# Performance work log

Hardware: AMD Instinct MI355X
Metric: run time of the kernel (lower is better)

Reference implementation:

```python
import jax, jax.numpy as jnp
import numpy as np

LN_EPS = 1e-5

def _layernorm(x, w, b):
    mu = jnp.mean(x, axis=-1, keepdims=True)
    var = jnp.mean(jnp.square(x - mu), axis=-1, keepdims=True)
    return (x - mu) * jax.lax.rsqrt(var + LN_EPS) * w + b

def setup_inputs() -> dict:
    key = jax.random.key(0)
    ks = jax.random.split(key, 6)
    B, NQ, QD = 8, 576, 4096
    NKV, KVD = 2304, 1024
    s = 0.02
    return {
        "x_q": jax.random.normal(ks[0], (B, NQ, QD), jnp.float32),
        "x_kv": jax.random.normal(ks[1], (B, NKV, KVD), jnp.float32),
        "q_ln_w": jnp.ones((QD,), jnp.float32),
        "q_ln_b": jnp.zeros((QD,), jnp.float32),
        "q_w": jax.random.normal(ks[2], (QD, QD), jnp.float32) * s,
        "q_b": jnp.zeros((QD,), jnp.float32),
        "k_ln_w": jnp.ones((KVD,), jnp.float32),
        "k_ln_b": jnp.zeros((KVD,), jnp.float32),
        "k_w": jax.random.normal(ks[3], (KVD, QD), jnp.float32) * s,
        "k_b": jnp.zeros((QD,), jnp.float32),
        "v_ln_w": jnp.ones((KVD,), jnp.float32),
        "v_ln_b": jnp.zeros((KVD,), jnp.float32),
        "v_w": jax.random.normal(ks[4], (KVD, QD), jnp.float32) * s,
        "v_b": jnp.zeros((QD,), jnp.float32),
    }

def reference(x_q, x_kv, q_ln_w, q_ln_b, q_w, q_b,
              k_ln_w, k_ln_b, k_w, k_b, v_ln_w, v_ln_b, v_w, v_b):
    B, NQ, QD = x_q.shape
    hw = int(round(x_kv.shape[1] ** 0.5))          # 48
    KVD = x_kv.shape[-1]
    patch_num = int(round(NQ ** 0.5))              # 24
    patch_size = hw // patch_num                   # 2
    # 'b (h w) d -> b h w d' then group into patch_num x patch_num windows
    kv = x_kv.reshape(B, hw, hw, KVD)
    kv = kv.reshape(B, patch_num, patch_size, patch_num, patch_size, KVD)
    kv = kv.transpose(0, 1, 3, 2, 4, 5).reshape(B, patch_num * patch_num, patch_size * patch_size, KVD)
    # projections (LayerNorm + Linear)
    q = _layernorm(x_q, q_ln_w, q_ln_b) @ q_w + q_b            # [B, P2, QD]
    k = _layernorm(kv, k_ln_w, k_ln_b) @ k_w + k_b             # [B, P2, S2, QD]
    v = _layernorm(kv, v_ln_w, v_ln_b) @ v_w + v_b             # [B, P2, S2, QD]
    scale = 1.0 / (QD ** 0.5)
    att = jnp.einsum('bpd,bpsd->bps', q, k) * scale            # [B, P2, S2]
    att = jnp.nan_to_num(att)
    att = jax.nn.softmax(att, axis=-1)
    feat = jnp.einsum('bps,bpsd->bpd', att, v)                 # [B, P2, QD]
    return (x_q, feat)
```

## Files before the change

kernel.cpp:

```cpp
#include <hip/hip_runtime.h>
#include <cstdint>
#include <cstddef>


typedef __attribute__((ext_vector_type(8))) short short8;
typedef __attribute__((ext_vector_type(4))) float f32x4;

#define DEV __device__ __forceinline__

DEV unsigned short f2bf(float f) {
  union { float f; unsigned u; } x; x.f = f;
  unsigned r = x.u + 0x7fffu + ((x.u >> 16) & 1u);
  return (unsigned short)(r >> 16);
}
DEV float bf2f(unsigned short u) {
  union { unsigned u; float f; } x; x.u = ((unsigned)u) << 16;
  return x.f;
}

DEV void gload16(const void* g, void* l) {
  __builtin_amdgcn_global_load_lds(
      (const __attribute__((address_space(1))) unsigned int*)g,
      (__attribute__((address_space(3))) unsigned int*)l, 16, 0, 0);
}

template <bool PARTIAL, bool OUT_BF16, bool HAS_BIAS>
__global__ __launch_bounds__(256, 2) void gemm_nt(
    const unsigned short* __restrict__ A, const unsigned short* __restrict__ Bm,
    void* __restrict__ Cv, const float* __restrict__ bias, int M, int N,
    int Kfull, int Kchunk) {
  __shared__ __align__(16) unsigned short lds_a[128 * 64];
  __shared__ __align__(16) unsigned short lds_b[128 * 64];
  const int t = threadIdx.x;
  const int l = t & 63;
  const int w = t >> 6;

  int bx = blockIdx.x, by = blockIdx.y;
  {
    const int nbx = gridDim.x, nby = gridDim.y;
    const int nwg = nbx * nby;
    int flat = by * nbx + bx;
    flat = (flat & 7) * (nwg >> 3) + (flat >> 3);
    bx = flat % nbx;
    by = flat / nbx;
  }
  const long brow = (long)bx * 128;
  const long bcol = (long)by * 128;
  const int z = blockIdx.z;
  const int k0 = z * Kchunk;

  const int srow0 = t >> 3;
  const int gsrc = (t & 7) ^ ((t >> 3) & 7);
  const unsigned short* aS[4];
  const unsigned short* bS[4];
  unsigned short* aD[4];
  unsigned short* bD[4];
#pragma unroll
  for (int j = 0; j < 4; ++j) {
    const long row = srow0 + 32 * j;
    aS[j] = A + (brow + row) * (long)Kfull + k0 + gsrc * 8;
    bS[j] = Bm + (bcol + row) * (long)Kfull + k0 + gsrc * 8;
    aD[j] = lds_a + (t + 256 * j) * 8;
    bD[j] = lds_b + (t + 256 * j) * 8;
  }

  const int wr = w >> 1, wc = w & 1;
  const int fr = l & 15;
  const int xr = fr & 7;
  const int gq0 = l >> 4;

  f32x4 acc[4][4] = {};

  for (int kt = 0; kt < Kchunk; kt += 64) {
    __syncthreads();
#pragma unroll
    for (int j = 0; j < 4; ++j) {
      gload16(aS[j] + kt, aD[j]);
      gload16(bS[j] + kt, bD[j]);
    }
    asm volatile("s_waitcnt vmcnt(0)" ::: "memory");
    __syncthreads();
#pragma unroll
    for (int ks = 0; ks < 2; ++ks) {
      const int gx = ((ks * 4 + gq0) ^ xr) * 8;
      short8 af[4], bfr[4];
#pragma unroll
      for (int mi = 0; mi < 4; ++mi)
        af[mi] = *(const short8*)&lds_a[(wr * 64 + mi * 16 + fr) * 64 + gx];
#pragma unroll
      for (int ni = 0; ni < 4; ++ni)
        bfr[ni] = *(const short8*)&lds_b[(wc * 64 + ni * 16 + fr) * 64 + gx];
#pragma unroll
      for (int mi = 0; mi < 4; ++mi)
#pragma unroll
        for (int ni = 0; ni < 4; ++ni)
          acc[mi][ni] = __builtin_amdgcn_mfma_f32_16x16x32_bf16(
              af[mi], bfr[ni], acc[mi][ni], 0, 0, 0);
    }
  }

  const int crow = (l >> 4) * 4;
  float* Cpart = PARTIAL ? ((float*)Cv + (size_t)z * M * (size_t)N) : nullptr;
#pragma unroll
  for (int ni = 0; ni < 4; ++ni) {
    const long col = bcol + wc * 64 + ni * 16 + fr;
    const float bv = (!PARTIAL && HAS_BIAS) ? bias[col] : 0.0f;
#pragma unroll
    for (int mi = 0; mi < 4; ++mi) {
#pragma unroll
      for (int r = 0; r < 4; ++r) {
        const long row = brow + wr * 64 + mi * 16 + crow + r;
        const float v = acc[mi][ni][r] + bv;
        if (PARTIAL)
          Cpart[row * (long)N + col] = v;
        else if (OUT_BF16)
          ((unsigned short*)Cv)[row * (long)N + col] = f2bf(v);
        else
          ((float*)Cv)[row * (long)N + col] = v;
      }
    }
  }
}

__global__ __launch_bounds__(256) void reduce_splits_bf16(
    const float* __restrict__ part, unsigned short* __restrict__ out, int S,
    size_t MN) {
  size_t i = (size_t)blockIdx.x * 256 + threadIdx.x;
  const size_t n4 = MN / 4;
  const size_t stride = (size_t)gridDim.x * 256;
  for (; i < n4; i += stride) {
    float4 a = ((const float4*)part)[i];
    for (int s = 1; s < S; ++s) {
      const float4 b = ((const float4*)(part + (size_t)s * MN))[i];
      a.x += b.x; a.y += b.y; a.z += b.z; a.w += b.w;
    }
    ((ushort4*)out)[i] =
        make_ushort4(f2bf(a.x), f2bf(a.y), f2bf(a.z), f2bf(a.w));
  }
}

__global__ __launch_bounds__(256) void ln_q_kernel(
    const float* __restrict__ x, const float* __restrict__ w,
    const float* __restrict__ b, float* __restrict__ copy_out,
    unsigned short* __restrict__ qn) {
  const int row = blockIdx.x, t = threadIdx.x;
  const float4* xr = (const float4*)(x + (size_t)row * 4096);
  float4 v[4];
  float s = 0.f, s2 = 0.f;
#pragma unroll
  for (int j = 0; j < 4; ++j) {
    v[j] = xr[j * 256 + t];
    s += v[j].x + v[j].y + v[j].z + v[j].w;
    s2 += v[j].x * v[j].x + v[j].y * v[j].y + v[j].z * v[j].z + v[j].w * v[j].w;
  }
#pragma unroll
  for (int off = 32; off; off >>= 1) {
    s += __shfl_xor(s, off);
    s2 += __shfl_xor(s2, off);
  }
  __shared__ float red[8];
  if ((t & 63) == 0) { red[t >> 6] = s; red[4 + (t >> 6)] = s2; }
  __syncthreads();
  s = red[0] + red[1] + red[2] + red[3];
  s2 = red[4] + red[5] + red[6] + red[7];
  const float mu = s * (1.f / 4096.f);
  const float rstd = rsqrtf(s2 * (1.f / 4096.f) - mu * mu + 1e-5f);
  float4* co = (float4*)(copy_out + (size_t)row * 4096);
  unsigned short* qr = qn + (size_t)row * 4096;
#pragma unroll
  for (int j = 0; j < 4; ++j) {
    co[j * 256 + t] = v[j];
    const int c = (j * 256 + t) * 4;
    const float4 wv = *(const float4*)(w + c);
    const float4 bv = *(const float4*)(b + c);
    ushort4 o = make_ushort4(f2bf((v[j].x - mu) * rstd * wv.x + bv.x),
                             f2bf((v[j].y - mu) * rstd * wv.y + bv.y),
                             f2bf((v[j].z - mu) * rstd * wv.z + bv.z),
                             f2bf((v[j].w - mu) * rstd * wv.w + bv.w));
    *(ushort4*)(qr + c) = o;
  }
}

__global__ __launch_bounds__(256) void ln_kv_kernel(
    const float* __restrict__ x, const float* __restrict__ kw,
    const float* __restrict__ kb, const float* __restrict__ vw,
    const float* __restrict__ vb, unsigned short* __restrict__ kn,
    unsigned short* __restrict__ vn) {
  const int row = blockIdx.x, t = threadIdx.x;
  const float4 v = ((const float4*)(x + (size_t)row * 1024))[t];
  float s = v.x + v.y + v.z + v.w;
  float s2 = v.x * v.x + v.y * v.y + v.z * v.z + v.w * v.w;
#pragma unroll
  for (int off = 32; off; off >>= 1) {
    s += __shfl_xor(s, off);
    s2 += __shfl_xor(s2, off);
  }
  __shared__ float red[8];
  if ((t & 63) == 0) { red[t >> 6] = s; red[4 + (t >> 6)] = s2; }
  __syncthreads();
  s = red[0] + red[1] + red[2] + red[3];
  s2 = red[4] + red[5] + red[6] + red[7];
  const float mu = s * (1.f / 1024.f);
  const float rstd = rsqrtf(s2 * (1.f / 1024.f) - mu * mu + 1e-5f);
  const int c = t * 4;
  const float4 kw4 = *(const float4*)(kw + c);
  const float4 kb4 = *(const float4*)(kb + c);
  const float4 vw4 = *(const float4*)(vw + c);
  const float4 vb4 = *(const float4*)(vb + c);
  const float h0 = (v.x - mu) * rstd, h1 = (v.y - mu) * rstd;
  const float h2 = (v.z - mu) * rstd, h3 = (v.w - mu) * rstd;
  *(ushort4*)(kn + (size_t)row * 1024 + c) =
      make_ushort4(f2bf(h0 * kw4.x + kb4.x), f2bf(h1 * kw4.y + kb4.y),
                   f2bf(h2 * kw4.z + kb4.z), f2bf(h3 * kw4.w + kb4.w));
  *(ushort4*)(vn + (size_t)row * 1024 + c) =
      make_ushort4(f2bf(h0 * vw4.x + vb4.x), f2bf(h1 * vw4.y + vb4.y),
                   f2bf(h2 * vw4.z + vb4.z), f2bf(h3 * vw4.w + vb4.w));
}

__global__ __launch_bounds__(256) void conv_bf16(
    const float* __restrict__ src, unsigned short* __restrict__ dst, int n4) {
  int i = blockIdx.x * 256 + threadIdx.x;
  const int stride = gridDim.x * 256;
  for (; i < n4; i += stride) {
    const float4 v = ((const float4*)src)[i];
    ((ushort4*)dst)[i] = make_ushort4(f2bf(v.x), f2bf(v.y), f2bf(v.z), f2bf(v.w));
  }
}

__global__ void transpose_conv(const float* __restrict__ src,
                               unsigned short* __restrict__ dst) {
  __shared__ float tile[32][33];
  const int n0 = blockIdx.x * 32, k0 = blockIdx.y * 32;
  const int tx = threadIdx.x, ty = threadIdx.y;
#pragma unroll
  for (int i = 0; i < 32; i += 8)
    tile[ty + i][tx] = src[(size_t)(k0 + ty + i) * 4096 + n0 + tx];
  __syncthreads();
#pragma unroll
  for (int i = 0; i < 32; i += 8)
    dst[(size_t)(n0 + ty + i) * 1024 + k0 + tx] = f2bf(tile[tx][ty + i]);
}

__global__ __launch_bounds__(256) void qkb_kernel(const float* __restrict__ qb,
                                                  const float* __restrict__ kw,
                                                  float* __restrict__ out) {
  const int c = blockIdx.x, t = threadIdx.x;
  const float4* kr = (const float4*)(kw + (size_t)c * 4096);
  const float4* q4 = (const float4*)qb;
  float s = 0.f;
#pragma unroll
  for (int j = 0; j < 4; ++j) {
    const float4 a = q4[j * 256 + t], b = kr[j * 256 + t];
    s += a.x * b.x + a.y * b.y + a.z * b.z + a.w * b.w;
  }
#pragma unroll
  for (int off = 32; off; off >>= 1) s += __shfl_xor(s, off);
  __shared__ float red[4];
  if ((t & 63) == 0) red[t >> 6] = s;
  __syncthreads();
  if (t == 0) out[c] = red[0] + red[1] + red[2] + red[3];
}

__global__ __launch_bounds__(256) void att_fused(
    const float* __restrict__ part, int S, size_t PMN,
    const float* __restrict__ qkb, const unsigned short* __restrict__ kn,
    const unsigned short* __restrict__ vn, unsigned short* __restrict__ wkv) {
  const int m = blockIdx.x;
  const int b = m / 576, p = m % 576;
  const int py = p / 24, px = p % 24;
  const int t = threadIdx.x, w = t >> 6, l = t & 63;
  const int c = t * 4;
  const size_t off = (size_t)m * 1024 + c;

  float4 q = *(const float4*)(part + off);
  for (int s = 1; s < S; ++s) {
    const float4 pp = *(const float4*)(part + (size_t)s * PMN + off);
    q.x += pp.x; q.y += pp.y; q.z += pp.z; q.w += pp.w;
  }
  const float4 qb4 = *(const float4*)(qkb + c);
  q.x += qb4.x; q.y += qb4.y; q.z += qb4.z; q.w += qb4.w;

  size_t rows[4];
#pragma unroll
  for (int s = 0; s < 4; ++s)
    rows[s] = ((size_t)b * 2304 + (size_t)(py * 2 + (s >> 1)) * 48 +
               (px * 2 + (s & 1))) * 1024;

  float dot[4];
#pragma unroll
  for (int s = 0; s < 4; ++s) {
    const ushort4 k4 = *(const ushort4*)(kn + rows[s] + c);
    dot[s] = q.x * bf2f(k4.x) + q.y * bf2f(k4.y) + q.z * bf2f(k4.z) +
             q.w * bf2f(k4.w);
  }
#pragma unroll
  for (int s = 0; s < 4; ++s)
#pragma unroll
    for (int o = 32; o; o >>= 1) dot[s] += __shfl_xor(dot[s], o);

  __shared__ float red[4][4];
  if (l == 0) {
#pragma unroll
    for (int s = 0; s < 4; ++s) red[w][s] = dot[s];
  }
  __syncthreads();
  float lg[4];
#pragma unroll
  for (int s = 0; s < 4; ++s)
    lg[s] = (red[0][s] + red[1][s] + red[2][s] + red[3][s]) * 0.015625f;
  const float mx = fmaxf(fmaxf(lg[0], lg[1]), fmaxf(lg[2], lg[3]));
  float e[4];
#pragma unroll
  for (int s = 0; s < 4; ++s) e[s] = __expf(lg[s] - mx);
  const float inv = 1.f / (e[0] + e[1] + e[2] + e[3]);

  float a0 = 0.f, a1 = 0.f, a2 = 0.f, a3 = 0.f;
#pragma unroll
  for (int s = 0; s < 4; ++s) {
    const float at = e[s] * inv;
    const ushort4 v4 = *(const ushort4*)(vn + rows[s] + c);
    a0 += at * bf2f(v4.x);
    a1 += at * bf2f(v4.y);
    a2 += at * bf2f(v4.z);
    a3 += at * bf2f(v4.w);
  }
  *(ushort4*)(wkv + off) =
      make_ushort4(f2bf(a0), f2bf(a1), f2bf(a2), f2bf(a3));
}

extern "C" void kernel_launch(void* const* d_in, const int* in_sizes, int n_in,
                              void* d_out, int out_size, void* d_ws,
                              size_t ws_size, hipStream_t stream) {
  const float* x_q = (const float*)d_in[0];
  const float* x_kv = (const float*)d_in[1];
  const float* q_ln_w = (const float*)d_in[2];
  const float* q_ln_b = (const float*)d_in[3];
  const float* q_w = (const float*)d_in[4];
  const float* q_b = (const float*)d_in[5];
  const float* k_ln_w = (const float*)d_in[6];
  const float* k_ln_b = (const float*)d_in[7];
  const float* k_w = (const float*)d_in[8];
  const float* v_ln_w = (const float*)d_in[10];
  const float* v_ln_b = (const float*)d_in[11];
  const float* v_w = (const float*)d_in[12];
  const float* v_b = (const float*)d_in[13];

  char* ws = (char*)d_ws;
  unsigned short* qn = (unsigned short*)(ws);
  unsigned short* kn = (unsigned short*)(ws + 37748736);
  unsigned short* vn = (unsigned short*)(ws + 75497472);
  unsigned short* qwb = (unsigned short*)(ws + 113246208);
  unsigned short* kwb = (unsigned short*)(ws + 146800640);
  unsigned short* Wt = (unsigned short*)(ws + 155189248);
  unsigned short* vwT = (unsigned short*)(ws + 163577856);
  float* qkbv = (float*)(ws + 190840832);
  unsigned short* wkv = (unsigned short*)(ws + 190844928);
  float* part = (float*)(ws + 200282112);

  const size_t MN_W = (size_t)1024 * 4096;
  const size_t MN_QK = (size_t)4608 * 1024;
  int splitW = 1, splitQK = 1;
  if (ws_size >= 200282112ull + 4 * MN_QK * 4) { splitW = 2; splitQK = 4; }
  else if (ws_size >= 200282112ull + 2 * MN_QK * 4) { splitW = 2; splitQK = 2; }

  float* out0 = (float*)d_out;
  float* out1 = out0 + (size_t)4608 * 4096;

  ln_q_kernel<<<4608, 256, 0, stream>>>(x_q, q_ln_w, q_ln_b, out0, qn);
  ln_kv_kernel<<<18432, 256, 0, stream>>>(x_kv, k_ln_w, k_ln_b, v_ln_w, v_ln_b,
                                          kn, vn);
  conv_bf16<<<4096, 256, 0, stream>>>(q_w, qwb, 4096 * 4096 / 4);
  conv_bf16<<<1024, 256, 0, stream>>>(k_w, kwb, 1024 * 4096 / 4);
  transpose_conv<<<dim3(128, 32), dim3(32, 8), 0, stream>>>(v_w, vwT);
  qkb_kernel<<<1024, 256, 0, stream>>>(q_b, k_w, qkbv);

  gemm_nt<true, false, false><<<dim3(8, 32, splitW), 256, 0, stream>>>(
      kwb, qwb, part, nullptr, 1024, 4096, 4096, 4096 / splitW);
  reduce_splits_bf16<<<2048, 256, 0, stream>>>(part, Wt, splitW, MN_W);

  gemm_nt<true, false, false><<<dim3(36, 8, splitQK), 256, 0, stream>>>(
      qn, Wt, part, nullptr, 4608, 1024, 4096, 4096 / splitQK);
  att_fused<<<4608, 256, 0, stream>>>(part, splitQK, MN_QK, qkbv, kn, vn, wkv);

  gemm_nt<false, false, true><<<dim3(36, 32), 256, 0, stream>>>(
      wkv, vwT, out1, v_b, 4608, 4096, 1024, 1024);
}
```

Baseline: 560.5 us.

## Double-buffer GEMM LDS tiles, fuse k_w conversion with qkb, reduce QK split

The GEMM main loop now double-buffers its LDS tiles. The next K tile's global-to-LDS loads are issued before the MFMAs on the current tile, and wave priority is raised around the MFMA block, so memory latency can overlap compute. The k_w bf16 conversion and the q_b·k_w bias dot product now share one kernel instead of reading k_w twice in two launches. The QK GEMM split-K drops from 4 to 2, which cuts partial-sum traffic but leaves fewer workgroups. Doubling LDS to 64KB per block may reduce occupancy under the launch bound of 2.

Result: slower. 592.0 us (+5.6%).

```diff
diff --git a/kernel.cpp b/kernel.cpp
--- a/kernel.cpp
+++ b/kernel.cpp
@@ -29,8 +29,8 @@
     const unsigned short* __restrict__ A, const unsigned short* __restrict__ Bm,
     void* __restrict__ Cv, const float* __restrict__ bias, int M, int N,
     int Kfull, int Kchunk) {
-  __shared__ __align__(16) unsigned short lds_a[128 * 64];
-  __shared__ __align__(16) unsigned short lds_b[128 * 64];
+  __shared__ __align__(16) unsigned short lds_a[2][128 * 64];
+  __shared__ __align__(16) unsigned short lds_b[2][128 * 64];
   const int t = threadIdx.x;
   const int l = t & 63;
   const int w = t >> 6;
@@ -53,16 +53,13 @@
   const int gsrc = (t & 7) ^ ((t >> 3) & 7);
   const unsigned short* aS[4];
   const unsigned short* bS[4];
-  unsigned short* aD[4];
-  unsigned short* bD[4];
 #pragma unroll
   for (int j = 0; j < 4; ++j) {
     const long row = srow0 + 32 * j;
     aS[j] = A + (brow + row) * (long)Kfull + k0 + gsrc * 8;
     bS[j] = Bm + (bcol + row) * (long)Kfull + k0 + gsrc * 8;
-    aD[j] = lds_a + (t + 256 * j) * 8;
-    bD[j] = lds_b + (t + 256 * j) * 8;
-  }
+  }
+  const int dOff = t * 8;
 
   const int wr = w >> 1, wc = w & 1;
   const int fr = l & 15;
@@ -71,32 +68,46 @@
 
   f32x4 acc[4][4] = {};
 
+#pragma unroll
+  for (int j = 0; j < 4; ++j) {
+    gload16(aS[j], &lds_a[0][dOff + 2048 * j]);
+    gload16(bS[j], &lds_b[0][dOff + 2048 * j]);
+  }
+  asm volatile("s_waitcnt vmcnt(0)" ::: "memory");
+  __syncthreads();
+
+  int cur = 0;
   for (int kt = 0; kt < Kchunk; kt += 64) {
-    __syncthreads();
-#pragma unroll
-    for (int j = 0; j < 4; ++j) {
-      gload16(aS[j] + kt, aD[j]);
-      gload16(bS[j] + kt, bD[j]);
+    const int nxt = cur ^ 1;
+    if (kt + 64 < Kchunk) {
+#pragma unroll
+      for (int j = 0; j < 4; ++j) {
+        gload16(aS[j] + kt + 64, &lds_a[nxt][dOff + 2048 * j]);
+        gload16(bS[j] + kt + 64, &lds_b[nxt][dOff + 2048 * j]);
+      }
+    }
+#pragma unroll
+    for (int ks = 0; ks < 2; ++ks) {
+      const int gx = ((ks * 4 + gq0) ^ xr) * 8;
+      short8 af[4], bfr[4];
+#pragma unroll
+      for (int mi = 0; mi < 4; ++mi)
+        af[mi] = *(const short8*)&lds_a[cur][(wr * 64 + mi * 16 + fr) * 64 + gx];
+#pragma unroll
+      for (int ni = 0; ni < 4; ++ni)
+        bfr[ni] = *(const short8*)&lds_b[cur][(wc * 64 + ni * 16 + fr) * 64 + gx];
+      __builtin_amdgcn_s_setprio(1);
+#pragma unroll
+      for (int mi = 0; mi < 4; ++mi)
+#pragma unroll
+        for (int ni = 0; ni < 4; ++ni)
+          acc[mi][ni] = __builtin_amdgcn_mfma_f32_16x16x32_bf16(
+              af[mi], bfr[ni], acc[mi][ni], 0, 0, 0);
+      __builtin_amdgcn_s_setprio(0);
     }
     asm volatile("s_waitcnt vmcnt(0)" ::: "memory");
     __syncthreads();
-#pragma unroll
-    for (int ks = 0; ks < 2; ++ks) {
-      const int gx = ((ks * 4 + gq0) ^ xr) * 8;
-      short8 af[4], bfr[4];
-#pragma unroll
-      for (int mi = 0; mi < 4; ++mi)
-        af[mi] = *(const short8*)&lds_a[(wr * 64 + mi * 16 + fr) * 64 + gx];
-#pragma unroll
-      for (int ni = 0; ni < 4; ++ni)
-        bfr[ni] = *(const short8*)&lds_b[(wc * 64 + ni * 16 + fr) * 64 + gx];
-#pragma unroll
-      for (int mi = 0; mi < 4; ++mi)
-#pragma unroll
-        for (int ni = 0; ni < 4; ++ni)
-          acc[mi][ni] = __builtin_amdgcn_mfma_f32_16x16x32_bf16(
-              af[mi], bfr[ni], acc[mi][ni], 0, 0, 0);
-    }
+    cur = nxt;
   }
 
   const int crow = (l >> 4) * 4;
@@ -227,6 +238,28 @@
   }
 }
 
+__global__ __launch_bounds__(256) void conv_kw_qkb(
+    const float* __restrict__ kw, const float* __restrict__ qb,
+    unsigned short* __restrict__ kwb, float* __restrict__ qkb) {
+  const int c = blockIdx.x, t = threadIdx.x;
+  const float4* kr = (const float4*)(kw + (size_t)c * 4096);
+  const float4* q4 = (const float4*)qb;
+  ushort4* ko = (ushort4*)(kwb + (size_t)c * 4096);
+  float s = 0.f;
+#pragma unroll
+  for (int j = 0; j < 4; ++j) {
+    const float4 a = q4[j * 256 + t], b = kr[j * 256 + t];
+    ko[j * 256 + t] = make_ushort4(f2bf(b.x), f2bf(b.y), f2bf(b.z), f2bf(b.w));
+    s += a.x * b.x + a.y * b.y + a.z * b.z + a.w * b.w;
+  }
+#pragma unroll
+  for (int off = 32; off; off >>= 1) s += __shfl_xor(s, off);
+  __shared__ float red[4];
+  if ((t & 63) == 0) red[t >> 6] = s;
+  __syncthreads();
+  if (t == 0) qkb[c] = red[0] + red[1] + red[2] + red[3];
+}
+
 __global__ void transpose_conv(const float* __restrict__ src,
                                unsigned short* __restrict__ dst) {
   __shared__ float tile[32][33];
@@ -239,26 +272,6 @@
 #pragma unroll
   for (int i = 0; i < 32; i += 8)
     dst[(size_t)(n0 + ty + i) * 1024 + k0 + tx] = f2bf(tile[tx][ty + i]);
-}
-
-__global__ __launch_bounds__(256) void qkb_kernel(const float* __restrict__ qb,
-                                                  const float* __restrict__ kw,
-                                                  float* __restrict__ out) {
-  const int c = blockIdx.x, t = threadIdx.x;
-  const float4* kr = (const float4*)(kw + (size_t)c * 4096);
-  const float4* q4 = (const float4*)qb;
-  float s = 0.f;
-#pragma unroll
-  for (int j = 0; j < 4; ++j) {
-    const float4 a = q4[j * 256 + t], b = kr[j * 256 + t];
-    s += a.x * b.x + a.y * b.y + a.z * b.z + a.w * b.w;
-  }
-#pragma unroll
-  for (int off = 32; off; off >>= 1) s += __shfl_xor(s, off);
-  __shared__ float red[4];
-  if ((t & 63) == 0) red[t >> 6] = s;
-  __syncthreads();
-  if (t == 0) out[c] = red[0] + red[1] + red[2] + red[3];
 }
 
 __global__ __launch_bounds__(256) void att_fused(
@@ -360,8 +373,7 @@
   const size_t MN_W = (size_t)1024 * 4096;
   const size_t MN_QK = (size_t)4608 * 1024;
   int splitW = 1, splitQK = 1;
-  if (ws_size >= 200282112ull + 4 * MN_QK * 4) { splitW = 2; splitQK = 4; }
-  else if (ws_size >= 200282112ull + 2 * MN_QK * 4) { splitW = 2; splitQK = 2; }
+  if (ws_size >= 200282112ull + 2 * MN_QK * 4) { splitW = 2; splitQK = 2; }
 
   float* out0 = (float*)d_out;
   float* out1 = out0 + (size_t)4608 * 4096;
@@ -370,9 +382,8 @@
   ln_kv_kernel<<<18432, 256, 0, stream>>>(x_kv, k_ln_w, k_ln_b, v_ln_w, v_ln_b,
                                           kn, vn);
   conv_bf16<<<4096, 256, 0, stream>>>(q_w, qwb, 4096 * 4096 / 4);
-  conv_bf16<<<1024, 256, 0, stream>>>(k_w, kwb, 1024 * 4096 / 4);
+  conv_kw_qkb<<<1024, 256, 0, stream>>>(k_w, q_b, kwb, qkbv);
   transpose_conv<<<dim3(128, 32), dim3(32, 8), 0, stream>>>(v_w, vwT);
-  qkb_kernel<<<1024, 256, 0, stream>>>(q_b, k_w, qkbv);
 
   gemm_nt<true, false, false><<<dim3(8, 32, splitW), 256, 0, stream>>>(
       kwb, qwb, part, nullptr, 1024, 4096, 4096, 4096 / splitW);
```
